# Kernel tuning notes

Measured on AMD Instinct MI355X. Metric: run time of the kernel, lower is better.

## Reference

```python
import jax, jax.numpy as jnp
import numpy as np

HIDDEN = 4096
NUM_EXPERTS = 64
TOKENS = 16384
TOP_K = 2


def setup_inputs() -> dict:
    key = jax.random.key(0)
    kx, kw = jax.random.split(key)
    x = jax.random.normal(kx, (TOKENS, HIDDEN), dtype=jnp.float32)
    # router gate weight, as in nn.Parameter(torch.randn(num_experts, hidden_size))
    weight = jax.random.normal(kw, (NUM_EXPERTS, HIDDEN), dtype=jnp.float32)
    return {"x": x, "weight": weight}


def reference(x, weight):
    # logits = F.linear(x, weight)  -> [tokens, num_experts]
    logits = jnp.einsum("th,eh->te", x, weight)
    # top-2 experts per token, then softmax over the 2 selected logits
    top_vals, selected_experts = jax.lax.top_k(logits, TOP_K)  # [tokens, 2]
    weights = jax.nn.softmax(top_vals, axis=-1)
    return weights, selected_experts
```

## Files before the change

### kernel.cpp

```cpp
#include <hip/hip_runtime.h>
#include <math.h>

#define TOKENS 16384
#define HIDDEN 4096
#define NEXP   64
#define TOKB   32
#define WAVES  4
#define KSL    (HIDDEN / WAVES)
#define NCH    (KSL / 32)

typedef _Float16 half8 __attribute__((ext_vector_type(8)));
typedef float    f32x4 __attribute__((ext_vector_type(4)));

__global__ void w_prep(const float* __restrict__ W,
                       _Float16* __restrict__ Wh, _Float16* __restrict__ Wl) {
    int idx = blockIdx.x * blockDim.x + threadIdx.x;
    int e = idx >> 12;
    int k = idx & 4095;
    float v = W[idx];
    _Float16 h = (_Float16)v;
    _Float16 l = (_Float16)(v - (float)h);
    size_t dst = (((size_t)(k >> 5) * NEXP) + e) * 32 + (k & 31);
    Wh[dst] = h;
    Wl[dst] = l;
}

__device__ __forceinline__ void split8(const float4& p0, const float4& p1,
                                       half8& h, half8& l) {
    const float v[8] = {p0.x, p0.y, p0.z, p0.w, p1.x, p1.y, p1.z, p1.w};
    #pragma unroll
    for (int j = 0; j < 8; ++j) {
        _Float16 hi = (_Float16)v[j];
        h[j] = hi;
        l[j] = (_Float16)(v[j] - (float)hi);
    }
}

__global__ __launch_bounds__(256, 2) void router_fused(
    const float* __restrict__ x, const _Float16* __restrict__ Wh,
    const _Float16* __restrict__ Wl, float* __restrict__ out)
{
    __shared__ float lds[WAVES][NEXP][36];

    const int tid  = threadIdx.x;
    const int lane = tid & 63;
    const int wv   = tid >> 6;
    const int e16  = lane & 15;
    const int quad = lane >> 4;

    const int tok0 = blockIdx.x * TOKB;
    const int kb0  = wv * NCH;

    f32x4 accA[4], accB[4];
    #pragma unroll
    for (int n = 0; n < 4; ++n) {
        accA[n] = (f32x4){0.f, 0.f, 0.f, 0.f};
        accB[n] = (f32x4){0.f, 0.f, 0.f, 0.f};
    }

    const float* xpA = x + (size_t)(tok0 + e16) * HIDDEN + wv * KSL + quad * 8;
    const float* xpB = xpA + (size_t)16 * HIDDEN;

    float4 pA0 = *(const float4*)(xpA),     pA1 = *(const float4*)(xpA + 4);
    float4 pB0 = *(const float4*)(xpB),     pB1 = *(const float4*)(xpB + 4);

    for (int c = 0; c < NCH; ++c) {
        const size_t bo = (((size_t)(kb0 + c) * NEXP) + e16) * 32 + quad * 8;
        half8 bh[4], bl[4];
        #pragma unroll
        for (int n = 0; n < 4; ++n) {
            bh[n] = *reinterpret_cast<const half8*>(Wh + bo + (size_t)n * 16 * 32);
            bl[n] = *reinterpret_cast<const half8*>(Wl + bo + (size_t)n * 16 * 32);
        }

        half8 ahA, alA, ahB, alB;
        split8(pA0, pA1, ahA, alA);
        split8(pB0, pB1, ahB, alB);
        if (c + 1 < NCH) {
            pA0 = *(const float4*)(xpA + (c + 1) * 32);
            pA1 = *(const float4*)(xpA + (c + 1) * 32 + 4);
            pB0 = *(const float4*)(xpB + (c + 1) * 32);
            pB1 = *(const float4*)(xpB + (c + 1) * 32 + 4);
        }

        #pragma unroll
        for (int n = 0; n < 4; ++n)
            accA[n] = __builtin_amdgcn_mfma_f32_16x16x32_f16(alA, bh[n], accA[n], 0, 0, 0);
        #pragma unroll
        for (int n = 0; n < 4; ++n)
            accB[n] = __builtin_amdgcn_mfma_f32_16x16x32_f16(alB, bh[n], accB[n], 0, 0, 0);
        #pragma unroll
        for (int n = 0; n < 4; ++n)
            accA[n] = __builtin_amdgcn_mfma_f32_16x16x32_f16(ahA, bl[n], accA[n], 0, 0, 0);
        #pragma unroll
        for (int n = 0; n < 4; ++n)
            accB[n] = __builtin_amdgcn_mfma_f32_16x16x32_f16(ahB, bl[n], accB[n], 0, 0, 0);
        #pragma unroll
        for (int n = 0; n < 4; ++n)
            accA[n] = __builtin_amdgcn_mfma_f32_16x16x32_f16(ahA, bh[n], accA[n], 0, 0, 0);
        #pragma unroll
        for (int n = 0; n < 4; ++n)
            accB[n] = __builtin_amdgcn_mfma_f32_16x16x32_f16(ahB, bh[n], accB[n], 0, 0, 0);
    }

    #pragma unroll
    for (int n = 0; n < 4; ++n) {
        *(f32x4*)&lds[wv][n * 16 + e16][quad * 4]      = accA[n];
        *(f32x4*)&lds[wv][n * 16 + e16][16 + quad * 4] = accB[n];
    }
    __syncthreads();

    {
        const int e = tid >> 2;
        const int q = tid & 3;
        f32x4 s0 = (f32x4){0.f, 0.f, 0.f, 0.f};
        f32x4 s1 = (f32x4){0.f, 0.f, 0.f, 0.f};
        #pragma unroll
        for (int w = 0; w < WAVES; ++w) {
            s0 += *(const f32x4*)&lds[w][e][q * 8];
            s1 += *(const f32x4*)&lds[w][e][q * 8 + 4];
        }
        *(f32x4*)&lds[0][e][q * 8]     = s0;
        *(f32x4*)&lds[0][e][q * 8 + 4] = s1;
    }
    __syncthreads();

    if (tid < TOKB) {
        float v1 = -INFINITY, v2 = -INFINITY;
        int i1 = 0, i2 = 0;
        #pragma unroll 8
        for (int e = 0; e < NEXP; ++e) {
            float v = lds[0][e][tid];
            if (v > v1)      { v2 = v1; i2 = i1; v1 = v; i1 = e; }
            else if (v > v2) { v2 = v;  i2 = e; }
        }
        float e2 = expf(v2 - v1);
        float d  = 1.f / (1.f + e2);
        int t = tok0 + tid;
        out[t * 2 + 0] = d;
        out[t * 2 + 1] = e2 * d;
        out[2 * TOKENS + t * 2 + 0] = (float)i1;
        out[2 * TOKENS + t * 2 + 1] = (float)i2;
    }
}

extern "C" void kernel_launch(void* const* d_in, const int* in_sizes, int n_in,
                              void* d_out, int out_size, void* d_ws, size_t ws_size,
                              hipStream_t stream) {
    const float* x = (const float*)d_in[0];
    const float* W = (const float*)d_in[1];
    float* out = (float*)d_out;

    _Float16* Wh = (_Float16*)d_ws;
    _Float16* Wl = Wh + (size_t)NEXP * HIDDEN;

    w_prep<<<(NEXP * HIDDEN) / 256, 256, 0, stream>>>(W, Wh, Wl);
    router_fused<<<TOKENS / TOKB, 256, 0, stream>>>(x, Wh, Wl, out);
}
```

Before: 392.6 us.

## Fuse weight fp16 split into router kernel and deepen x prefetch

```diff
diff --git a/kernel.cpp b/kernel.cpp
--- a/kernel.cpp
+++ b/kernel.cpp
@@ -12,19 +12,6 @@
 typedef _Float16 half8 __attribute__((ext_vector_type(8)));
 typedef float    f32x4 __attribute__((ext_vector_type(4)));
 
-__global__ void w_prep(const float* __restrict__ W,
-                       _Float16* __restrict__ Wh, _Float16* __restrict__ Wl) {
-    int idx = blockIdx.x * blockDim.x + threadIdx.x;
-    int e = idx >> 12;
-    int k = idx & 4095;
-    float v = W[idx];
-    _Float16 h = (_Float16)v;
-    _Float16 l = (_Float16)(v - (float)h);
-    size_t dst = (((size_t)(k >> 5) * NEXP) + e) * 32 + (k & 31);
-    Wh[dst] = h;
-    Wl[dst] = l;
-}
-
 __device__ __forceinline__ void split8(const float4& p0, const float4& p1,
                                        half8& h, half8& l) {
     const float v[8] = {p0.x, p0.y, p0.z, p0.w, p1.x, p1.y, p1.z, p1.w};
@@ -37,8 +24,8 @@
 }
 
 __global__ __launch_bounds__(256, 2) void router_fused(
-    const float* __restrict__ x, const _Float16* __restrict__ Wh,
-    const _Float16* __restrict__ Wl, float* __restrict__ out)
+    const float* __restrict__ x, const float* __restrict__ W,
+    float* __restrict__ out)
 {
     __shared__ float lds[WAVES][NEXP][36];
 
@@ -47,9 +34,7 @@
     const int wv   = tid >> 6;
     const int e16  = lane & 15;
     const int quad = lane >> 4;
-
     const int tok0 = blockIdx.x * TOKB;
-    const int kb0  = wv * NCH;
 
     f32x4 accA[4], accB[4];
     #pragma unroll
@@ -60,48 +45,74 @@
 
     const float* xpA = x + (size_t)(tok0 + e16) * HIDDEN + wv * KSL + quad * 8;
     const float* xpB = xpA + (size_t)16 * HIDDEN;
+    const float* wp  = W + (size_t)e16 * HIDDEN + wv * KSL + quad * 8;
 
-    float4 pA0 = *(const float4*)(xpA),     pA1 = *(const float4*)(xpA + 4);
-    float4 pB0 = *(const float4*)(xpB),     pB1 = *(const float4*)(xpB + 4);
+    float4 a00 = *(const float4*)(xpA),      a01 = *(const float4*)(xpA + 4);
+    float4 b00 = *(const float4*)(xpB),      b01 = *(const float4*)(xpB + 4);
+    float4 a10 = *(const float4*)(xpA + 32), a11 = *(const float4*)(xpA + 36);
+    float4 b10 = *(const float4*)(xpB + 32), b11 = *(const float4*)(xpB + 36);
 
-    for (int c = 0; c < NCH; ++c) {
-        const size_t bo = (((size_t)(kb0 + c) * NEXP) + e16) * 32 + quad * 8;
-        half8 bh[4], bl[4];
-        #pragma unroll
-        for (int n = 0; n < 4; ++n) {
-            bh[n] = *reinterpret_cast<const half8*>(Wh + bo + (size_t)n * 16 * 32);
-            bl[n] = *reinterpret_cast<const half8*>(Wl + bo + (size_t)n * 16 * 32);
-        }
+    float4 w0[4], w1[4];
+    #pragma unroll
+    for (int n = 0; n < 4; ++n) {
+        w0[n] = *(const float4*)(wp + (size_t)n * 16 * HIDDEN);
+        w1[n] = *(const float4*)(wp + (size_t)n * 16 * HIDDEN + 4);
+    }
 
-        half8 ahA, alA, ahB, alB;
-        split8(pA0, pA1, ahA, alA);
-        split8(pB0, pB1, ahB, alB);
-        if (c + 1 < NCH) {
-            pA0 = *(const float4*)(xpA + (c + 1) * 32);
-            pA1 = *(const float4*)(xpA + (c + 1) * 32 + 4);
-            pB0 = *(const float4*)(xpB + (c + 1) * 32);
-            pB1 = *(const float4*)(xpB + (c + 1) * 32 + 4);
-        }
+#define CHUNK_BODY(c, A0, A1, B0, B1)                                          \
+    {                                                                          \
+        half8 bh[4], bl[4];                                                    \
+        _Pragma("unroll")                                                      \
+        for (int n = 0; n < 4; ++n) split8(w0[n], w1[n], bh[n], bl[n]);        \
+        if ((c) + 1 < NCH) {                                                   \
+            _Pragma("unroll")                                                  \
+            for (int n = 0; n < 4; ++n) {                                      \
+                w0[n] = *(const float4*)(wp + (size_t)n * 16 * HIDDEN          \
+                                             + ((c) + 1) * 32);                \
+                w1[n] = *(const float4*)(wp + (size_t)n * 16 * HIDDEN          \
+                                             + ((c) + 1) * 32 + 4);            \
+            }                                                                  \
+        }                                                                      \
+        half8 ahA, alA, ahB, alB;                                              \
+        split8(A0, A1, ahA, alA);                                              \
+        split8(B0, B1, ahB, alB);                                              \
+        if ((c) + 2 < NCH) {                                                   \
+            A0 = *(const float4*)(xpA + ((c) + 2) * 32);                       \
+            A1 = *(const float4*)(xpA + ((c) + 2) * 32 + 4);                   \
+            B0 = *(const float4*)(xpB + ((c) + 2) * 32);                       \
+            B1 = *(const float4*)(xpB + ((c) + 2) * 32 + 4);                   \
+        }                                                                      \
+        _Pragma("unroll")                                                      \
+        for (int n = 0; n < 4; ++n)                                            \
+            accA[n] = __builtin_amdgcn_mfma_f32_16x16x32_f16(alA, bh[n],       \
+                                                             accA[n], 0, 0, 0);\
+        _Pragma("unroll")                                                      \
+        for (int n = 0; n < 4; ++n)                                            \
+            accB[n] = __builtin_amdgcn_mfma_f32_16x16x32_f16(alB, bh[n],       \
+                                                             accB[n], 0, 0, 0);\
+        _Pragma("unroll")                                                      \
+        for (int n = 0; n < 4; ++n)                                            \
+            accA[n] = __builtin_amdgcn_mfma_f32_16x16x32_f16(ahA, bl[n],       \
+                                                             accA[n], 0, 0, 0);\
+        _Pragma("unroll")                                                      \
+        for (int n = 0; n < 4; ++n)                                            \
+            accB[n] = __builtin_amdgcn_mfma_f32_16x16x32_f16(ahB, bl[n],       \
+                                                             accB[n], 0, 0, 0);\
+        _Pragma("unroll")                                                      \
+        for (int n = 0; n < 4; ++n)                                            \
+            accA[n] = __builtin_amdgcn_mfma_f32_16x16x32_f16(ahA, bh[n],       \
+                                                             accA[n], 0, 0, 0);\
+        _Pragma("unroll")                                                      \
+        for (int n = 0; n < 4; ++n)                                            \
+            accB[n] = __builtin_amdgcn_mfma_f32_16x16x32_f16(ahB, bh[n],       \
+                                                             accB[n], 0, 0, 0);\
+    }
 
-        #pragma unroll
-        for (int n = 0; n < 4; ++n)
-            accA[n] = __builtin_amdgcn_mfma_f32_16x16x32_f16(alA, bh[n], accA[n], 0, 0, 0);
-        #pragma unroll
-        for (int n = 0; n < 4; ++n)
-            accB[n] = __builtin_amdgcn_mfma_f32_16x16x32_f16(alB, bh[n], accB[n], 0, 0, 0);
-        #pragma unroll
-        for (int n = 0; n < 4; ++n)
-            accA[n] = __builtin_amdgcn_mfma_f32_16x16x32_f16(ahA, bl[n], accA[n], 0, 0, 0);
-        #pragma unroll
-        for (int n = 0; n < 4; ++n)
-            accB[n] = __builtin_amdgcn_mfma_f32_16x16x32_f16(ahB, bl[n], accB[n], 0, 0, 0);
-        #pragma unroll
-        for (int n = 0; n < 4; ++n)
-            accA[n] = __builtin_amdgcn_mfma_f32_16x16x32_f16(ahA, bh[n], accA[n], 0, 0, 0);
-        #pragma unroll
-        for (int n = 0; n < 4; ++n)
-            accB[n] = __builtin_amdgcn_mfma_f32_16x16x32_f16(ahB, bh[n], accB[n], 0, 0, 0);
+    for (int c = 0; c < NCH; c += 2) {
+        CHUNK_BODY(c,     a00, a01, b00, b01);
+        CHUNK_BODY(c + 1, a10, a11, b10, b11);
     }
+#undef CHUNK_BODY
 
     #pragma unroll
     for (int n = 0; n < 4; ++n) {
@@ -150,10 +161,7 @@
     const float* x = (const float*)d_in[0];
     const float* W = (const float*)d_in[1];
     float* out = (float*)d_out;
+    (void)d_ws; (void)ws_size;
 
-    _Float16* Wh = (_Float16*)d_ws;
-    _Float16* Wl = Wh + (size_t)NEXP * HIDDEN;
-
-    w_prep<<<(NEXP * HIDDEN) / 256, 256, 0, stream>>>(W, Wh, Wl);
-    router_fused<<<TOKENS / TOKB, 256, 0, stream>>>(x, Wh, Wl, out);
+    router_fused<<<TOKENS / TOKB, 256, 0, stream>>>(x, W, out);
 }
```

Result: no change. 391.2 us (-0.4%).
